# Kernel optimization log

Measured on AMD Instinct MI355X. Metric: run time of the kernel, lower is better.

The kernel has to match this reference:

```python
import jax, jax.numpy as jnp
import numpy as np

HEADS = 16


def setup_inputs() -> dict:
    key = jax.random.key(0)
    ks = jax.random.split(key, 5)
    n, s, d = 2, 2048, 1024
    return {
        "x": jax.random.normal(ks[0], (n, s, d), dtype=jnp.float32),
        "Wqkv": jax.random.normal(ks[1], (3 * d, d), dtype=jnp.float32) * (d ** -0.5),
        "bqkv": jax.random.normal(ks[2], (3 * d,), dtype=jnp.float32) * 0.02,
        "Wd": jax.random.normal(ks[3], (d, d), dtype=jnp.float32) * (d ** -0.5),
        "bd": jax.random.normal(ks[4], (d,), dtype=jnp.float32) * 0.02,
        "mask": 1,
    }


def reference(x, Wqkv, bqkv, Wd, bd, mask):
    n, s, d = x.shape
    h = HEADS
    hd = d // h
    qkv = x @ Wqkv.T + bqkv  # [n, s, 3d]
    q, k, v = jnp.split(qkv, 3, axis=-1)
    # [n, h, s, hd]
    q = q.reshape(n, s, h, hd).transpose(0, 2, 1, 3)
    k = k.reshape(n, s, h, hd).transpose(0, 2, 1, 3)
    v = v.reshape(n, s, h, hd).transpose(0, 2, 1, 3)
    scores = jnp.einsum("bhqd,bhkd->bhqk", q, k)
    if mask:
        causal = jnp.triu(jnp.ones((s, s), dtype=bool), k=1)
        scores = jnp.where(causal, -jnp.inf, scores)
    attn = jax.nn.softmax(scores / jnp.sqrt(jnp.float32(hd)), axis=-1)
    out = jnp.einsum("bhqk,bhkd->bhqd", attn, v)
    out = out.transpose(0, 2, 1, 3).reshape(n, s, d)
    return out @ Wd.T + bd
```

## Files before the change

kernel.cpp:

```cpp
#include <hip/hip_runtime.h>
#include <hip/hip_bf16.h>
#include <cstdint>
#include <cstddef>

typedef __attribute__((ext_vector_type(8))) short bf8_t;
typedef __attribute__((ext_vector_type(4))) float f4_t;

__device__ __forceinline__ unsigned short f2bf(float f) {
    union { float f; unsigned int u; } v; v.f = f;
    unsigned int u = v.u + 0x7FFFu + ((v.u >> 16) & 1u);
    return (unsigned short)(u >> 16);
}
__device__ __forceinline__ float bf2f(unsigned short s) {
    union { unsigned int u; float f; } v; v.u = ((unsigned int)s) << 16;
    return v.f;
}

__device__ __forceinline__ void gl_lds16(const void* g, void* l) {
    __builtin_amdgcn_global_load_lds(
        (const __attribute__((address_space(1))) unsigned int*)g,
        (__attribute__((address_space(3))) unsigned int*)l,
        16, 0, 0);
}

__global__ void cvt_kernel(const float* __restrict__ x,    unsigned short* __restrict__ xb,
                           const float* __restrict__ wq,   unsigned short* __restrict__ wqb,
                           const float* __restrict__ wd,   unsigned short* __restrict__ wdb) {
    int i = blockIdx.x * blockDim.x + threadIdx.x;
    const float* src; unsigned short* dst; int off;
    if (i < 1048576)       { src = x;  dst = xb;  off = i; }
    else if (i < 1835008)  { src = wq; dst = wqb; off = i - 1048576; }
    else                   { src = wd; dst = wdb; off = i - 1835008; }
    float4 f = ((const float4*)src)[off];
    ushort4 o;
    o.x = f2bf(f.x); o.y = f2bf(f.y); o.z = f2bf(f.z); o.w = f2bf(f.w);
    ((ushort4*)dst)[off] = o;
}

template<int MODE, int TM>
__device__ __forceinline__ void gemm_body(
    const unsigned short* __restrict__ A,
    const unsigned short* __restrict__ W,
    const float* __restrict__ bias,
    float* __restrict__ outf,
    unsigned short* __restrict__ qb,
    unsigned short* __restrict__ kb,
    unsigned short* __restrict__ vtb,
    int K, int Nn)
{
    constexpr int HM = TM / 2;
    constexpr int MB = HM / 16;
    constexpr int AI = TM / 32;
    constexpr int SSTG = (TM + 128) * 64;
    constexpr int SMEM = (MODE == 0 && SSTG < 128 * 136) ? 128 * 136 : SSTG;

    __shared__ unsigned short smem[SMEM];
    unsigned short* As = smem;
    unsigned short* Bs = smem + TM * 64;

    const int tid  = threadIdx.x;
    const int lane = tid & 63;
    const int w    = tid >> 6;
    const int wm   = w & 1;
    const int wn   = w >> 1;
    const int quad = lane >> 4;
    const int l16  = lane & 15;
    const int m0   = blockIdx.y * TM;
    const int n0   = blockIdx.x * 128;

    const int lrow = lane >> 3;
    const int lcol = ((lane & 7) ^ lrow) << 3;

    f4_t acc[MB][4];
    {
        f4_t z = {0.f, 0.f, 0.f, 0.f};
        #pragma unroll
        for (int i = 0; i < MB; ++i)
            #pragma unroll
            for (int j = 0; j < 4; ++j) acc[i][j] = z;
    }

    const unsigned short* Agp = A + (size_t)(m0 + w * (TM / 4) + lrow) * K + lcol;
    const unsigned short* Bgp = W + (size_t)(n0 + w * 32 + lrow) * K + lcol;
    unsigned short* lAp = &As[(w * (TM / 4)) * 64];
    unsigned short* lBp = &Bs[(w * 32) * 64];

    for (int kk = 0; kk < K; kk += 64) {
        __syncthreads();
        #pragma unroll
        for (int i = 0; i < AI; ++i)
            gl_lds16(Agp + (size_t)(i * 8) * K + kk, lAp + i * 8 * 64);
        #pragma unroll
        for (int i = 0; i < 4; ++i)
            gl_lds16(Bgp + (size_t)(i * 8) * K + kk, lBp + i * 8 * 64);
        __syncthreads();

        const int sw = l16 & 7;
        #pragma unroll
        for (int ks = 0; ks < 2; ++ks) {
            bf8_t af[MB], bfr[4];
            #pragma unroll
            for (int mb = 0; mb < MB; ++mb)
                af[mb] = *(const bf8_t*)&As[(wm * HM + mb * 16 + l16) * 64 + ((((ks << 2) | quad) ^ sw) << 3)];
            #pragma unroll
            for (int nb = 0; nb < 4; ++nb)
                bfr[nb] = *(const bf8_t*)&Bs[(wn * 64 + nb * 16 + l16) * 64 + ((((ks << 2) | quad) ^ sw) << 3)];
            #pragma unroll
            for (int mb = 0; mb < MB; ++mb)
                #pragma unroll
                for (int nb = 0; nb < 4; ++nb)
                    acc[mb][nb] = __builtin_amdgcn_mfma_f32_16x16x32_bf16(af[mb], bfr[nb], acc[mb][nb], 0, 0, 0);
        }
    }

    if (MODE == 0 && n0 >= 2048) {
        unsigned short* T = smem;
        __syncthreads();
        #pragma unroll
        for (int nb = 0; nb < 4; ++nb) {
            const int colL = wn * 64 + nb * 16 + l16;
            const float bc = bias[n0 + colL];
            #pragma unroll
            for (int mb = 0; mb < MB; ++mb) {
                const int rowL = wm * HM + mb * 16 + quad * 4;
                uint2 p;
                p.x = (unsigned int)f2bf(acc[mb][nb][0] + bc) |
                      ((unsigned int)f2bf(acc[mb][nb][1] + bc) << 16);
                p.y = (unsigned int)f2bf(acc[mb][nb][2] + bc) |
                      ((unsigned int)f2bf(acc[mb][nb][3] + bc) << 16);
                *(uint2*)&T[colL * 136 + rowL] = p;
            }
        }
        __syncthreads();
        const int trow  = tid >> 1;
        const int thalf = (tid & 1) << 6;
        const int head  = ((n0 - 2048) >> 6) + (trow >> 6);
        const int hdi   = trow & 63;
        const int bh    = ((m0 >> 11) << 4) + head;
        const int sq0   = (m0 & 2047) + thalf;
        unsigned short* dst = vtb + ((size_t)bh * 64 + hdi) * 2048 + sq0;
        const unsigned short* srcT = &T[trow * 136 + thalf];
        #pragma unroll
        for (int j = 0; j < 8; ++j)
            *(float4*)(dst + j * 8) = *(const float4*)(srcT + j * 8);
        return;
    }

    #pragma unroll
    for (int nb = 0; nb < 4; ++nb) {
        const int col = n0 + wn * 64 + nb * 16 + l16;
        const float bc = bias[col];
        const int within = col & 1023;
        const int head   = within >> 6;
        const int hdi    = within & 63;
        const bool isQ   = (col < 1024);
        #pragma unroll
        for (int mb = 0; mb < MB; ++mb) {
            #pragma unroll
            for (int r = 0; r < 4; ++r) {
                const int row = m0 + wm * HM + mb * 16 + quad * 4 + r;
                const float v = acc[mb][nb][r] + bc;
                if (MODE == 0) {
                    const int b  = row >> 11;
                    const int sq = row & 2047;
                    const int bh = b * 16 + head;
                    const unsigned short bv = f2bf(v);
                    if (isQ) qb[((size_t)bh * 2048 + sq) * 64 + hdi] = bv;
                    else     kb[((size_t)bh * 2048 + sq) * 64 + hdi] = bv;
                } else {
                    outf[(size_t)row * Nn + col] = v;
                }
            }
        }
    }
}

__global__ __launch_bounds__(256, 2) void qkv_gemm(
    const unsigned short* __restrict__ A, const unsigned short* __restrict__ W,
    const float* __restrict__ bias, unsigned short* __restrict__ qb,
    unsigned short* __restrict__ kb, unsigned short* __restrict__ vtb, int K, int Nn)
{
    gemm_body<0, 128>(A, W, bias, nullptr, qb, kb, vtb, K, Nn);
}

__global__ __launch_bounds__(256, 2) void proj_gemm(
    const unsigned short* __restrict__ A, const unsigned short* __restrict__ W,
    const float* __restrict__ bias, float* __restrict__ outf, int K, int Nn)
{
    gemm_body<1, 64>(A, W, bias, outf, nullptr, nullptr, nullptr, K, Nn);
}

__global__ __launch_bounds__(256, 2) void attn_kernel(
    const unsigned short* __restrict__ qg,
    const unsigned short* __restrict__ kg,
    const unsigned short* __restrict__ vg,
    unsigned short* __restrict__ ao,
    unsigned short* __restrict__ pO,
    float* __restrict__ pL)
{
    __shared__ unsigned short Ks[2][4096];
    __shared__ unsigned short Vs[2][4096];
    __shared__ unsigned short Ps[8192];

    const int tid  = threadIdx.x;
    const int lane = tid & 63;
    const int w    = tid >> 6;
    const int quad = lane >> 4;
    const int l16  = lane & 15;
    const int bx   = blockIdx.x;
    const int bh   = ((bx & 7) << 2) | ((bx >> 3) & 3);
    const int rest = bx >> 5;
    const int jj   = rest & 7;
    const int h    = rest >> 3;
    const int qtBig   = 15 - jj;
    const int qtSmall = jj;
    const int b    = bh >> 4;
    const int head = bh & 15;
    const int p0len = 32 - 2 * jj;
    const int t0 = h ? 17 : 0;
    const int t1 = h ? 34 : 17;

    const unsigned short* Qp = qg + (size_t)bh * 2048 * 64;
    const unsigned short* Kp = kg + (size_t)bh * 2048 * 64;
    const unsigned short* Vp = vg + (size_t)bh * 64 * 2048;

    const int srow = lane >> 3;
    const int scol = ((lane & 7) ^ srow) << 3;
    const unsigned short* kga = Kp + (size_t)(w * 16 + srow) * 64 + scol;
    const unsigned short* vga = Vp + (size_t)(w * 16 + srow) * 2048 + scol;
    const int sw = l16 & 7;

    auto stageKV = [&](int kt, int buf) {
        const int sk0 = kt << 6;
        gl_lds16(kga + (size_t)sk0 * 64,       &Ks[buf][w * 16 * 64]);
        gl_lds16(kga + (size_t)sk0 * 64 + 512, &Ks[buf][(w * 16 + 8) * 64]);
        gl_lds16(vga + sk0,                    &Vs[buf][w * 16 * 64]);
        gl_lds16(vga + sk0 + 8 * 2048,         &Vs[buf][(w * 16 + 8) * 64]);
    };

    bf8_t bones;
    {
        const short one = (l16 == 0) ? (short)0x3F80 : (short)0;
        #pragma unroll
        for (int j = 0; j < 8; ++j) bones[j] = one;
    }

    f4_t oacc[2][4];
    f4_t lacc[2];
    {
        f4_t z = {0.f, 0.f, 0.f, 0.f};
        #pragma unroll
        for (int mb = 0; mb < 2; ++mb) {
            #pragma unroll
            for (int j = 0; j < 4; ++j) oacc[mb][j] = z;
            lacc[mb] = z;
        }
    }

    bf8_t aq[2][2];
    auto loadQ = [&](int qt) {
        const unsigned short* q0 = Qp + (size_t)(qt * 128 + w * 32 + l16) * 64 + quad * 8;
        aq[0][0] = *(const bf8_t*)(q0);
        aq[0][1] = *(const bf8_t*)(q0 + 32);
        aq[1][0] = *(const bf8_t*)(q0 + 16 * 64);
        aq[1][1] = *(const bf8_t*)(q0 + 16 * 64 + 32);
    };

    auto flushPartial = [&]() {
        const int tb = (h << 8) + (bh << 3) + jj;
        unsigned short* po = pO + (size_t)tb * 8192;
        #pragma unroll
        for (int mb = 0; mb < 2; ++mb)
            #pragma unroll
            for (int r = 0; r < 4; ++r) {
                const int row = w * 32 + mb * 16 + quad * 4 + r;
                #pragma unroll
                for (int nb = 0; nb < 4; ++nb)
                    po[row * 64 + nb * 16 + l16] = f2bf(oacc[mb][nb][r]);
                if (l16 == 0) pL[tb * 128 + row] = lacc[mb][r];
            }
    };

    loadQ(qtBig);

    stageKV((t0 >= p0len) ? (t0 - p0len) : t0, t0 & 1);

    for (int t = t0; t < t1; ++t) {
        const int buf = t & 1;
        __syncthreads();

        if (t + 1 < t1) {
            const int t2 = t + 1;
            stageKV((t2 >= p0len) ? (t2 - p0len) : t2, t2 & 1);
        }

        if (t == p0len) {
            flushPartial();
            f4_t z = {0.f, 0.f, 0.f, 0.f};
            #pragma unroll
            for (int mb = 0; mb < 2; ++mb) {
                #pragma unroll
                for (int j = 0; j < 4; ++j) oacc[mb][j] = z;
                lacc[mb] = z;
            }
            loadQ(qtSmall);
        }

        const bool ph1 = (t >= p0len);
        const int  kt  = ph1 ? (t - p0len) : t;
        const int  qtc = ph1 ? qtSmall : qtBig;
        const bool isD0 = (kt == 2 * qtc);
        const bool isD1 = (kt == 2 * qtc + 1);
        const bool diag = isD0 || isD1;
        const int  koff = isD1 ? 64 : 0;

        bf8_t bk[2][4];
        #pragma unroll
        for (int ks = 0; ks < 2; ++ks)
            #pragma unroll
            for (int nb = 0; nb < 4; ++nb)
                bk[ks][nb] = *(const bf8_t*)&Ks[buf][(nb * 16 + l16) * 64 + ((((ks << 2) | quad) ^ sw) << 3)];

        #pragma unroll
        for (int mb = 0; mb < 2; ++mb) {
            f4_t sacc[4];
            {
                f4_t z = {0.f, 0.f, 0.f, 0.f};
                #pragma unroll
                for (int j = 0; j < 4; ++j) sacc[j] = z;
            }
            #pragma unroll
            for (int ks = 0; ks < 2; ++ks)
                #pragma unroll
                for (int nb = 0; nb < 4; ++nb)
                    sacc[nb] = __builtin_amdgcn_mfma_f32_16x16x32_bf16(aq[mb][ks], bk[ks][nb], sacc[nb], 0, 0, 0);

            if (!diag) {
                #pragma unroll
                for (int r = 0; r < 4; ++r) {
                    const int rloc = w * 32 + mb * 16 + (quad << 2) + r;
                    const int rk = rloc & 7;
                    #pragma unroll
                    for (int nb = 0; nb < 4; ++nb) {
                        union { float f; unsigned int u; } pv;
                        pv.f = exp2f(fmaf(sacc[nb][r], 0.18033688f, -20.197731f));
                        Ps[rloc * 64 + ((((nb << 1) | (l16 >> 3)) ^ rk) << 3) + (l16 & 7)] =
                            (unsigned short)(pv.u >> 16);
                    }
                }
            } else {
                #pragma unroll
                for (int r = 0; r < 4; ++r) {
                    const int rloc = w * 32 + mb * 16 + (quad << 2) + r;
                    const int rk = rloc & 7;
                    #pragma unroll
                    for (int nb = 0; nb < 4; ++nb) {
                        float e = fmaf(sacc[nb][r], 0.18033688f, -20.197731f);
                        if (nb * 16 + l16 + koff > rloc) e = -1e30f;
                        union { float f; unsigned int u; } pv;
                        pv.f = exp2f(e);
                        Ps[rloc * 64 + ((((nb << 1) | (l16 >> 3)) ^ rk) << 3) + (l16 & 7)] =
                            (unsigned short)(pv.u >> 16);
                    }
                }
            }
        }

        bf8_t bv[2][4];
        #pragma unroll
        for (int ks = 0; ks < 2; ++ks)
            #pragma unroll
            for (int nb = 0; nb < 4; ++nb)
                bv[ks][nb] = *(const bf8_t*)&Vs[buf][(nb * 16 + l16) * 64 + ((((ks << 2) | quad) ^ sw) << 3)];

        #pragma unroll
        for (int mb = 0; mb < 2; ++mb)
            #pragma unroll
            for (int ks = 0; ks < 2; ++ks) {
                bf8_t ap = *(const bf8_t*)&Ps[(w * 32 + mb * 16 + l16) * 64 + ((((ks << 2) | quad) ^ sw) << 3)];
                #pragma unroll
                for (int nb = 0; nb < 4; ++nb)
                    oacc[mb][nb] = __builtin_amdgcn_mfma_f32_16x16x32_bf16(ap, bv[ks][nb], oacc[mb][nb], 0, 0, 0);
                lacc[mb] = __builtin_amdgcn_mfma_f32_16x16x32_bf16(ap, bones, lacc[mb], 0, 0, 0);
            }
    }

    if (!h) {
        flushPartial();
    } else {
        #pragma unroll
        for (int mb = 0; mb < 2; ++mb)
            #pragma unroll
            for (int r = 0; r < 4; ++r) {
                const float lsum = __shfl(lacc[mb][r], lane & 48);
                const float rl = 1.f / lsum;
                const int sq = qtSmall * 128 + w * 32 + mb * 16 + (quad << 2) + r;
                #pragma unroll
                for (int nb = 0; nb < 4; ++nb) {
                    const int dcol = head * 64 + nb * 16 + l16;
                    ao[((size_t)(b * 2048 + sq)) * 1024 + dcol] = f2bf(oacc[mb][nb][r] * rl);
                }
            }
    }
}

__global__ void merge_kernel(const unsigned short* __restrict__ pO,
                             const float* __restrict__ pL,
                             unsigned short* __restrict__ ao) {
    const int blk  = blockIdx.x;
    const int bh   = blk >> 3;
    const int jj   = blk & 7;
    const int b    = bh >> 4;
    const int head = bh & 15;
    const int qt   = 15 - jj;
    const int row  = threadIdx.x >> 1;
    const int c0   = (threadIdx.x & 1) << 5;

    const float l = pL[blk * 128 + row] + pL[(256 + blk) * 128 + row];
    const float rl = 1.f / l;
    const unsigned short* p0 = pO + (size_t)blk * 8192 + row * 64 + c0;
    const unsigned short* p1 = pO + (size_t)(256 + blk) * 8192 + row * 64 + c0;
    unsigned short* dst = ao + ((size_t)(b * 2048 + qt * 128 + row)) * 1024 + head * 64 + c0;
    #pragma unroll
    for (int j = 0; j < 32; ++j)
        dst[j] = f2bf((bf2f(p0[j]) + bf2f(p1[j])) * rl);
}

extern "C" void kernel_launch(void* const* d_in, const int* in_sizes, int n_in,
                              void* d_out, int out_size, void* d_ws, size_t ws_size,
                              hipStream_t stream) {
    const float* x    = (const float*)d_in[0];
    const float* Wqkv = (const float*)d_in[1];
    const float* bqkv = (const float*)d_in[2];
    const float* Wd   = (const float*)d_in[3];
    const float* bd   = (const float*)d_in[4];
    float* out = (float*)d_out;

    char* ws = (char*)d_ws;
    unsigned short* xb    = (unsigned short*)(ws);
    unsigned short* wqkvb = (unsigned short*)(ws + 8388608);
    unsigned short* wdb   = (unsigned short*)(ws + 14680064);
    unsigned short* qb2   = (unsigned short*)(ws + 16777216);
    unsigned short* kb2   = (unsigned short*)(ws + 25165824);
    unsigned short* vtb   = (unsigned short*)(ws + 33554432);
    unsigned short* pO    = (unsigned short*)(ws + 41943040);
    float*          pL    = (float*)(ws + 50331648);
    unsigned short* ao    = xb;

    cvt_kernel<<<8192, 256, 0, stream>>>(x, xb, Wqkv, wqkvb, Wd, wdb);

    qkv_gemm<<<dim3(24, 32), 256, 0, stream>>>(
        xb, wqkvb, bqkv, qb2, kb2, vtb, 1024, 3072);

    attn_kernel<<<512, 256, 0, stream>>>(qb2, kb2, vtb, ao, pO, pL);

    merge_kernel<<<256, 256, 0, stream>>>(pO, pL, ao);

    proj_gemm<<<dim3(8, 64), 256, 0, stream>>>(
        ao, wdb, bd, out, 1024, 1024);
}
```

Before: 175.1 us.

## Split attention KV work into three chunks per tile pair and merge partials

Each attention block's 34 KV steps are now split across three blocks instead of two, giving 768 blocks instead of 512. Every chunk writes unnormalized partials into four slots, and the merge kernel now handles both the big and small query tiles, summing two or three partials. Launch bounds are raised to three blocks per SIMD so the larger grid fits with better occupancy on the 256-CU device. The cost is more partial-output traffic and a larger merge, and the higher occupancy target may make registers spill.

New measurement: 268.5 us. 53.3% more time.

```diff
diff --git a/kernel.cpp b/kernel.cpp
--- a/kernel.cpp
+++ b/kernel.cpp
@@ -190,11 +190,10 @@
     gemm_body<1, 64>(A, W, bias, outf, nullptr, nullptr, nullptr, K, Nn);
 }
 
-__global__ __launch_bounds__(256, 2) void attn_kernel(
+__global__ __launch_bounds__(256, 3) void attn_kernel(
     const unsigned short* __restrict__ qg,
     const unsigned short* __restrict__ kg,
     const unsigned short* __restrict__ vg,
-    unsigned short* __restrict__ ao,
     unsigned short* __restrict__ pO,
     float* __restrict__ pL)
 {
@@ -211,14 +210,12 @@
     const int bh   = ((bx & 7) << 2) | ((bx >> 3) & 3);
     const int rest = bx >> 5;
     const int jj   = rest & 7;
-    const int h    = rest >> 3;
+    const int c    = rest >> 3;
     const int qtBig   = 15 - jj;
     const int qtSmall = jj;
-    const int b    = bh >> 4;
-    const int head = bh & 15;
     const int p0len = 32 - 2 * jj;
-    const int t0 = h ? 17 : 0;
-    const int t1 = h ? 34 : 17;
+    const int tA = (c == 0) ? 0  : (c == 1 ? 12 : 23);
+    const int tB = (c == 0) ? 12 : (c == 1 ? 23 : 34);
 
     const unsigned short* Qp = qg + (size_t)bh * 2048 * 64;
     const unsigned short* Kp = kg + (size_t)bh * 2048 * 64;
@@ -266,9 +263,10 @@
         aq[1][1] = *(const bf8_t*)(q0 + 16 * 64 + 32);
     };
 
-    auto flushPartial = [&]() {
-        const int tb = (h << 8) + (bh << 3) + jj;
-        unsigned short* po = pO + (size_t)tb * 8192;
+    auto flushPartial = [&](int slot) {
+        const int pair = (bh << 3) + jj;
+        unsigned short* po = pO + ((size_t)(slot << 8) + pair) * 8192;
+        float* pl = pL + ((slot << 8) + pair) * 128;
         #pragma unroll
         for (int mb = 0; mb < 2; ++mb)
             #pragma unroll
@@ -277,25 +275,25 @@
                 #pragma unroll
                 for (int nb = 0; nb < 4; ++nb)
                     po[row * 64 + nb * 16 + l16] = f2bf(oacc[mb][nb][r]);
-                if (l16 == 0) pL[tb * 128 + row] = lacc[mb][r];
+                if (l16 == 0) pl[row] = lacc[mb][r];
             }
     };
 
-    loadQ(qtBig);
-
-    stageKV((t0 >= p0len) ? (t0 - p0len) : t0, t0 & 1);
-
-    for (int t = t0; t < t1; ++t) {
+    loadQ((tA >= p0len) ? qtSmall : qtBig);
+
+    stageKV((tA >= p0len) ? (tA - p0len) : tA, tA & 1);
+
+    for (int t = tA; t < tB; ++t) {
         const int buf = t & 1;
         __syncthreads();
 
-        if (t + 1 < t1) {
+        if (t + 1 < tB) {
             const int t2 = t + 1;
             stageKV((t2 >= p0len) ? (t2 - p0len) : t2, t2 & 1);
         }
 
         if (t == p0len) {
-            flushPartial();
+            flushPartial(c == 1 ? 1 : 2);
             f4_t z = {0.f, 0.f, 0.f, 0.f};
             #pragma unroll
             for (int mb = 0; mb < 2; ++mb) {
@@ -385,45 +383,45 @@
             }
     }
 
-    if (!h) {
-        flushPartial();
-    } else {
-        #pragma unroll
-        for (int mb = 0; mb < 2; ++mb)
-            #pragma unroll
-            for (int r = 0; r < 4; ++r) {
-                const float lsum = __shfl(lacc[mb][r], lane & 48);
-                const float rl = 1.f / lsum;
-                const int sq = qtSmall * 128 + w * 32 + mb * 16 + (quad << 2) + r;
-                #pragma unroll
-                for (int nb = 0; nb < 4; ++nb) {
-                    const int dcol = head * 64 + nb * 16 + l16;
-                    ao[((size_t)(b * 2048 + sq)) * 1024 + dcol] = f2bf(oacc[mb][nb][r] * rl);
-                }
-            }
-    }
+    flushPartial(c == 0 ? 0 : (c == 1 ? (jj >= 5 ? 2 : 1) : 3));
 }
 
 __global__ void merge_kernel(const unsigned short* __restrict__ pO,
                              const float* __restrict__ pL,
                              unsigned short* __restrict__ ao) {
-    const int blk  = blockIdx.x;
-    const int bh   = blk >> 3;
-    const int jj   = blk & 7;
+    const int blk   = blockIdx.x;
+    const int pair  = blk >> 1;
+    const int phase = blk & 1;
+    const int bh   = pair >> 3;
+    const int jj   = pair & 7;
     const int b    = bh >> 4;
     const int head = bh & 15;
-    const int qt   = 15 - jj;
+    const int qt   = phase ? jj : (15 - jj);
     const int row  = threadIdx.x >> 1;
     const int c0   = (threadIdx.x & 1) << 5;
-
-    const float l = pL[blk * 128 + row] + pL[(256 + blk) * 128 + row];
+    const bool useS2 = phase ? (jj >= 5) : (jj <= 4);
+
+    const size_t pbase = (size_t)pair * 8192 + row * 64 + c0;
+    const int    lbase = pair * 128 + row;
+    constexpr size_t OS = 256 * 8192;
+    constexpr int    LS = 256 * 128;
+
+    float l;
+    if (phase == 0) l = pL[lbase] + pL[LS + lbase] + (useS2 ? pL[2 * LS + lbase] : 0.f);
+    else            l = pL[3 * LS + lbase] + (useS2 ? pL[2 * LS + lbase] : 0.f);
     const float rl = 1.f / l;
-    const unsigned short* p0 = pO + (size_t)blk * 8192 + row * 64 + c0;
-    const unsigned short* p1 = pO + (size_t)(256 + blk) * 8192 + row * 64 + c0;
+
+    const unsigned short* pA = pO + (phase ? 3 * OS : 0) + pbase;
+    const unsigned short* pB = pO + OS + pbase;
+    const unsigned short* p2 = pO + 2 * OS + pbase;
     unsigned short* dst = ao + ((size_t)(b * 2048 + qt * 128 + row)) * 1024 + head * 64 + c0;
     #pragma unroll
-    for (int j = 0; j < 32; ++j)
-        dst[j] = f2bf((bf2f(p0[j]) + bf2f(p1[j])) * rl);
+    for (int j = 0; j < 32; ++j) {
+        float v = bf2f(pA[j]);
+        if (phase == 0) v += bf2f(pB[j]);
+        if (useS2)      v += bf2f(p2[j]);
+        dst[j] = f2bf(v * rl);
+    }
 }
 
 extern "C" void kernel_launch(void* const* d_in, const int* in_sizes, int n_in,
@@ -444,7 +442,7 @@
     unsigned short* kb2   = (unsigned short*)(ws + 25165824);
     unsigned short* vtb   = (unsigned short*)(ws + 33554432);
     unsigned short* pO    = (unsigned short*)(ws + 41943040);
-    float*          pL    = (float*)(ws + 50331648);
+    float*          pL    = (float*)(ws + 58720256);
     unsigned short* ao    = xb;
 
     cvt_kernel<<<8192, 256, 0, stream>>>(x, xb, Wqkv, wqkvb, Wd, wdb);
@@ -452,9 +450,9 @@
     qkv_gemm<<<dim3(24, 32), 256, 0, stream>>>(
         xb, wqkvb, bqkv, qb2, kb2, vtb, 1024, 3072);
 
-    attn_kernel<<<512, 256, 0, stream>>>(qb2, kb2, vtb, ao, pO, pL);
-
-    merge_kernel<<<256, 256, 0, stream>>>(pO, pL, ao);
+    attn_kernel<<<768, 256, 0, stream>>>(qb2, kb2, vtb, pO, pL);
+
+    merge_kernel<<<512, 256, 0, stream>>>(pO, pL, ao);
 
     proj_gemm<<<dim3(8, 64), 256, 0, stream>>>(
         ao, wdb, bd, out, 1024, 1024);
```
